# Optimization experiments

Measured on AMD Instinct MI355X. Metric: run time of the kernel, lower is better.

## Reference

```python
import jax, jax.numpy as jnp
import numpy as np

BATCH = 2048          # options['batch_size']; 2B = 4096 rows
D = 512               # projection dim
TAU = 0.1             # options['tau']


def _neg_cols(bs):
    """Column indices of negatives per row, matching sim[mask].view(2bs, -1).

    mask excludes the main diagonal and the +/- bs off-diagonals; each row
    keeps 2bs-2 columns, in ascending (row-major) order.
    """
    n = 2 * bs
    mask = ~(np.eye(n, dtype=bool)
             | np.eye(n, k=bs, dtype=bool)
             | np.eye(n, k=-bs, dtype=bool))
    cols = np.nonzero(mask)[1].reshape(n, n - 2).astype(np.int32)
    return cols

_NEG_COLS = _neg_cols(BATCH)  # static (2B, 2B-2) int32 constant


def setup_inputs() -> dict:
    key = jax.random.key(0)
    representation = jax.random.normal(key, (2 * BATCH, D), dtype=jnp.float32)
    return {"representation": representation}


def reference(representation):
    bs = representation.shape[0] // 2
    # dot-product similarity (options['cosine_similarity'] == False)
    sim = representation @ representation.T                     # (2B, 2B)
    l_pos = jnp.diagonal(sim, offset=bs)                        # (B,)
    r_pos = jnp.diagonal(sim, offset=-bs)                       # (B,)
    positives = jnp.concatenate([l_pos, r_pos])[:, None]        # (2B, 1)
    negatives = jnp.take_along_axis(sim, jnp.asarray(_NEG_COLS), axis=1)  # (2B, 2B-2)
    logits = jnp.concatenate([positives, negatives], axis=1) / TAU
    # CrossEntropyLoss(reduction='sum') with all labels == 0, then / 2B
    loss = -jax.nn.log_softmax(logits, axis=-1)[:, 0]
    return jnp.sum(loss) / (2 * bs)
```

## Files before the change

### kernel.cpp

```cpp
#include <hip/hip_runtime.h>
#include <hip/hip_bf16.h>


#define NROWS 4096
#define DDIM  512
#define NSPLIT 16
#define NT 8
#define BM 128
#define NEG_BIG (-3.0e38f)
#define SQRT_CSCALE 3.798282562f
#define LN2 0.69314718055994530942f
#define THR 40.0f

typedef __bf16 bf16x8 __attribute__((ext_vector_type(8)));
typedef float  f32x4  __attribute__((ext_vector_type(4)));

#define GLOAD_LDS16(g, l) __builtin_amdgcn_global_load_lds(                    \
    (const __attribute__((address_space(1))) void*)(g),                        \
    (__attribute__((address_space(3))) void*)(l), 16, 0, 0)

#define MFMA16(a, b, c) __builtin_amdgcn_mfma_f32_16x16x32_bf16((a), (b), (c), 0, 0, 0)

__global__ void jl_cvt(const float* __restrict__ in, __bf16* __restrict__ out) {
    int i = (blockIdx.x * 256 + threadIdx.x) * 8;
    float4 a = *(const float4*)(in + i);
    float4 b = *(const float4*)(in + i + 4);
    bf16x8 w;
    w[0] = (__bf16)(a.x * SQRT_CSCALE); w[1] = (__bf16)(a.y * SQRT_CSCALE);
    w[2] = (__bf16)(a.z * SQRT_CSCALE); w[3] = (__bf16)(a.w * SQRT_CSCALE);
    w[4] = (__bf16)(b.x * SQRT_CSCALE); w[5] = (__bf16)(b.y * SQRT_CSCALE);
    w[6] = (__bf16)(b.z * SQRT_CSCALE); w[7] = (__bf16)(b.w * SQRT_CSCALE);
    *(bf16x8*)(out + i) = w;
}

__global__ __launch_bounds__(256, 2) void jl_main(const __bf16* __restrict__ rb,
                                                  float* __restrict__ pm,
                                                  float* __restrict__ ps,
                                                  float* __restrict__ pos) {
    __shared__ __align__(16) char smem[2][32][1024];

    const int rbk  = blockIdx.x >> 4;
    const int q    = blockIdx.x & 15;
    const int wave = threadIdx.x >> 6;
    const int lane = threadIdx.x & 63;

    const int row0 = rbk * BM + wave * 32;
    const int col0 = q * 256;
    const int lrow = lane & 15;
    const int lk   = lane >> 4;
    const int swz  = (lrow & 7) << 4;

    bf16x8 afA[16], afB[16];
    {
        const __bf16* arow = rb + (size_t)(row0 + lrow) * DDIM + lk * 8;
        #pragma unroll
        for (int kb = 0; kb < 16; ++kb) {
            afA[kb] = *(const bf16x8*)(arow + kb * 32);
            afB[kb] = *(const bf16x8*)(arow + 16 * DDIM + kb * 32);
        }
    }

#define STAGE(J)                                                               \
    do {                                                                       \
        _Pragma("unroll")                                                      \
        for (int i_ = 0; i_ < 8; ++i_) {                                       \
            const int rl_ = wave * 8 + i_;                                     \
            const char* g_ = (const char*)(rb + (size_t)(col0 + (J) * 32 + rl_) * DDIM) \
                             + ((lane * 16) ^ ((rl_ & 7) << 4));               \
            GLOAD_LDS16(g_, &smem[(J) & 1][rl_][0]);                           \
        }                                                                      \
    } while (0)

    STAGE(0);

    float m[2][4], s[2][4];
    #pragma unroll
    for (int h = 0; h < 2; ++h)
        #pragma unroll
        for (int r = 0; r < 4; ++r) { m[h][r] = NEG_BIG; s[h][r] = 0.0f; }

    for (int jt = 0; jt < NT; ++jt) {
        asm volatile("s_waitcnt vmcnt(0)" ::: "memory");
        __builtin_amdgcn_s_barrier();
        __builtin_amdgcn_sched_barrier(0);
        if (jt + 1 < NT) STAGE(jt + 1);

        const int cb = jt & 1;

        f32x4 a00 = {0.f,0.f,0.f,0.f}, a01 = {0.f,0.f,0.f,0.f};
        f32x4 a10 = {0.f,0.f,0.f,0.f}, a11 = {0.f,0.f,0.f,0.f};
        __builtin_amdgcn_s_setprio(1);
        #pragma unroll
        for (int kb = 0; kb < 16; ++kb) {
            bf16x8 b0 = *(const bf16x8*)(&smem[cb][lrow][0]      + ((kb * 64 + lk * 16) ^ swz));
            bf16x8 b1 = *(const bf16x8*)(&smem[cb][16 + lrow][0] + ((kb * 64 + lk * 16) ^ swz));
            a00 = MFMA16(afA[kb], b0, a00);
            a10 = MFMA16(afB[kb], b0, a10);
            a01 = MFMA16(afA[kb], b1, a01);
            a11 = MFMA16(afB[kb], b1, a11);
        }
        __builtin_amdgcn_s_setprio(0);

        f32x4 y[2][2] = {{a00, a01}, {a10, a11}};
        const int ctile = col0 + jt * 32;

        if (ctile == (row0 ^ 2048)) {
            #pragma unroll
            for (int h = 0; h < 2; ++h)
                #pragma unroll
                for (int r = 0; r < 4; ++r)
                    if (lrow == 4 * lk + r)
                        pos[row0 + h * 16 + 4 * lk + r] = y[h][h][r];
        }

        if (ctile == row0) {
            #pragma unroll
            for (int h = 0; h < 2; ++h)
                #pragma unroll
                for (int r = 0; r < 4; ++r) {
                    if (lrow == 4 * lk + r) y[h][h][r] = NEG_BIG;
                    float y0 = y[h][0][r], y1 = y[h][1][r];
                    float mn = fmaxf(m[h][r], fmaxf(y0, y1));
                    s[h][r] = s[h][r] * __builtin_amdgcn_exp2f(m[h][r] - mn)
                            + __builtin_amdgcn_exp2f(y0 - mn)
                            + __builtin_amdgcn_exp2f(y1 - mn);
                    m[h][r] = mn;
                }
        } else {
            float t[2][2][4];
            float dmax = NEG_BIG;
            #pragma unroll
            for (int h = 0; h < 2; ++h)
                #pragma unroll
                for (int n = 0; n < 2; ++n)
                    #pragma unroll
                    for (int r = 0; r < 4; ++r) {
                        t[h][n][r] = y[h][n][r] - m[h][r];
                        dmax = fmaxf(dmax, t[h][n][r]);
                    }
            if (__any(dmax > THR)) {
                #pragma unroll
                for (int h = 0; h < 2; ++h)
                    #pragma unroll
                    for (int r = 0; r < 4; ++r) {
                        float y0 = y[h][0][r], y1 = y[h][1][r];
                        float mn = fmaxf(m[h][r], fmaxf(y0, y1));
                        s[h][r] = s[h][r] * __builtin_amdgcn_exp2f(m[h][r] - mn)
                                + __builtin_amdgcn_exp2f(y0 - mn)
                                + __builtin_amdgcn_exp2f(y1 - mn);
                        m[h][r] = mn;
                    }
            } else {
                #pragma unroll
                for (int h = 0; h < 2; ++h)
                    #pragma unroll
                    for (int r = 0; r < 4; ++r)
                        s[h][r] += __builtin_amdgcn_exp2f(t[h][0][r])
                                 + __builtin_amdgcn_exp2f(t[h][1][r]);
            }
        }
    }
#undef STAGE

    #pragma unroll
    for (int h = 0; h < 2; ++h)
        #pragma unroll
        for (int r = 0; r < 4; ++r) {
            float mm = m[h][r], ss = s[h][r];
            #pragma unroll
            for (int off = 1; off < 16; off <<= 1) {
                float mo = __shfl_xor(mm, off, 64);
                float so = __shfl_xor(ss, off, 64);
                float mn = fmaxf(mm, mo);
                ss = ss * __builtin_amdgcn_exp2f(mm - mn)
                   + so * __builtin_amdgcn_exp2f(mo - mn);
                mm = mn;
            }
            if (lrow == 0) {
                const int grow = row0 + 16 * h + 4 * lk + r;
                pm[grow * NSPLIT + q] = mm;
                ps[grow * NSPLIT + q] = ss;
            }
        }
}

__global__ void jl_rowloss(const float* __restrict__ pm, const float* __restrict__ ps,
                           const float* __restrict__ pos, float* __restrict__ part) {
    __shared__ float red[256];
    const int t = threadIdx.x;
    const int row = blockIdx.x * 256 + t;
    float mb = NEG_BIG;
    #pragma unroll
    for (int qq = 0; qq < NSPLIT; ++qq) mb = fmaxf(mb, pm[row * NSPLIT + qq]);
    float st = 0.0f;
    #pragma unroll
    for (int qq = 0; qq < NSPLIT; ++qq)
        st += ps[row * NSPLIT + qq] * __builtin_amdgcn_exp2f(pm[row * NSPLIT + qq] - mb);
    red[t] = mb + __builtin_amdgcn_logf(st) - pos[row];
    __syncthreads();
    for (int off = 128; off > 0; off >>= 1) {
        if (t < off) red[t] += red[t + off];
        __syncthreads();
    }
    if (t == 0) part[blockIdx.x] = red[0];
}

__global__ void jl_final(const float* __restrict__ part, float* __restrict__ out) {
    const int t = threadIdx.x;
    float v = (t < NROWS / 256) ? part[t] : 0.0f;
    #pragma unroll
    for (int off = 1; off < 16; off <<= 1) v += __shfl_xor(v, off, 64);
    if (t == 0) out[0] = v * (LN2 / (float)NROWS);
}

extern "C" void kernel_launch(void* const* d_in, const int* in_sizes, int n_in,
                              void* d_out, int out_size, void* d_ws, size_t ws_size,
                              hipStream_t stream) {
    const float* rep = (const float*)d_in[0];
    float* out = (float*)d_out;

    __bf16* rbuf = (__bf16*)d_ws;
    float*  pm   = (float*)(rbuf + (size_t)NROWS * DDIM);
    float*  ps   = pm + NROWS * NSPLIT;
    float*  pos  = ps + NROWS * NSPLIT;
    float*  part = pos + NROWS;

    jl_cvt<<<(NROWS * DDIM) / (256 * 8), 256, 0, stream>>>(rep, rbuf);
    jl_main<<<32 * NSPLIT, 256, 0, stream>>>(rbuf, pm, ps, pos);
    jl_rowloss<<<NROWS / 256, 256, 0, stream>>>(pm, ps, pos, part);
    jl_final<<<1, 64, 0, stream>>>(part, out);
}
```

Measured before the change: 42.01 us.

## Restructure main kernel into 256x256 block tiles with K-streamed LDS staging

The main kernel switches from 128-row blocks that hold A fragments in registers and stream 32-column B tiles to 512-thread blocks computing full 256x256 output tiles. Both A and B are staged through double-buffered LDS in 64-wide K chunks, and each wave accumulates a 128x64 sub-tile. The online softmax now runs once after accumulation instead of per column tile. This raises arithmetic intensity per LDS byte and removes the per-tile softmax bookkeeping, at the cost of 128 accumulator registers per thread, 128 KB of LDS, extra barriers, and four times as many partial (max, sum) slots for the row-reduction kernel.

```diff
diff --git a/kernel.cpp b/kernel.cpp
--- a/kernel.cpp
+++ b/kernel.cpp
@@ -4,13 +4,10 @@
 
 #define NROWS 4096
 #define DDIM  512
-#define NSPLIT 16
-#define NT 8
-#define BM 128
+#define NSLOT 64
 #define NEG_BIG (-3.0e38f)
 #define SQRT_CSCALE 3.798282562f
 #define LN2 0.69314718055994530942f
-#define THR 40.0f
 
 typedef __bf16 bf16x8 __attribute__((ext_vector_type(8)));
 typedef float  f32x4  __attribute__((ext_vector_type(4)));
@@ -33,155 +30,137 @@
     *(bf16x8*)(out + i) = w;
 }
 
-__global__ __launch_bounds__(256, 2) void jl_main(const __bf16* __restrict__ rb,
+__global__ __launch_bounds__(512, 2) void jl_main(const __bf16* __restrict__ rb,
                                                   float* __restrict__ pm,
                                                   float* __restrict__ ps,
                                                   float* __restrict__ pos) {
-    __shared__ __align__(16) char smem[2][32][1024];
+    __shared__ __align__(16) char lds[2][2][256 * 128];
 
     const int rbk  = blockIdx.x >> 4;
     const int q    = blockIdx.x & 15;
     const int wave = threadIdx.x >> 6;
     const int lane = threadIdx.x & 63;
-
-    const int row0 = rbk * BM + wave * 32;
-    const int col0 = q * 256;
+    const int wr   = wave >> 2;
+    const int wc   = wave & 3;
     const int lrow = lane & 15;
     const int lk   = lane >> 4;
-    const int swz  = (lrow & 7) << 4;
-
-    bf16x8 afA[16], afB[16];
-    {
-        const __bf16* arow = rb + (size_t)(row0 + lrow) * DDIM + lk * 8;
+
+    const int row0 = rbk * 256;
+    const int col0 = q * 256;
+    const char* rbb = (const char*)rb;
+
+    const int srow = wave * 32 + (lane >> 3);
+    const int ssw  = ((lane & 7) << 4) ^ (((lane >> 3) & 7) << 4);
+    const char* gA = rbb + (size_t)(row0 + srow) * 1024 + ssw;
+    const char* gB = rbb + (size_t)(col0 + srow) * 1024 + ssw;
+
+#define STAGEP(T, i)                                                           \
+    do {                                                                       \
+        GLOAD_LDS16(gA + (size_t)(T) * 128 + (i) * 8192,                       \
+                    &lds[(T) & 1][0][(wave * 32 + 8 * (i)) * 128]);            \
+        GLOAD_LDS16(gB + (size_t)(T) * 128 + (i) * 8192,                       \
+                    &lds[(T) & 1][1][(wave * 32 + 8 * (i)) * 128]);            \
+    } while (0)
+
+    const int rswz = (lrow & 7) << 4;
+#define AOFF(fr, kb) (((wr * 128 + (fr) * 16 + lrow) * 128) + ((((kb) * 64) + lk * 16) ^ rswz))
+#define BOFF(fc, kb) (((wc * 64 + (fc) * 16 + lrow) * 128) + ((((kb) * 64) + lk * 16) ^ rswz))
+
+    f32x4 acc[8][4];
+    #pragma unroll
+    for (int fr = 0; fr < 8; ++fr)
         #pragma unroll
-        for (int kb = 0; kb < 16; ++kb) {
-            afA[kb] = *(const bf16x8*)(arow + kb * 32);
-            afB[kb] = *(const bf16x8*)(arow + 16 * DDIM + kb * 32);
-        }
-    }
-
-#define STAGE(J)                                                               \
-    do {                                                                       \
-        _Pragma("unroll")                                                      \
-        for (int i_ = 0; i_ < 8; ++i_) {                                       \
-            const int rl_ = wave * 8 + i_;                                     \
-            const char* g_ = (const char*)(rb + (size_t)(col0 + (J) * 32 + rl_) * DDIM) \
-                             + ((lane * 16) ^ ((rl_ & 7) << 4));               \
-            GLOAD_LDS16(g_, &smem[(J) & 1][rl_][0]);                           \
-        }                                                                      \
-    } while (0)
-
-    STAGE(0);
-
-    float m[2][4], s[2][4];
-    #pragma unroll
-    for (int h = 0; h < 2; ++h)
-        #pragma unroll
-        for (int r = 0; r < 4; ++r) { m[h][r] = NEG_BIG; s[h][r] = 0.0f; }
-
-    for (int jt = 0; jt < NT; ++jt) {
+        for (int fc = 0; fc < 4; ++fc)
+            acc[fr][fc] = (f32x4){0.f, 0.f, 0.f, 0.f};
+
+    #pragma unroll
+    for (int i = 0; i < 4; ++i) STAGEP(0, i);
+
+    for (int t = 0; t < 8; ++t) {
         asm volatile("s_waitcnt vmcnt(0)" ::: "memory");
         __builtin_amdgcn_s_barrier();
         __builtin_amdgcn_sched_barrier(0);
-        if (jt + 1 < NT) STAGE(jt + 1);
-
-        const int cb = jt & 1;
-
-        f32x4 a00 = {0.f,0.f,0.f,0.f}, a01 = {0.f,0.f,0.f,0.f};
-        f32x4 a10 = {0.f,0.f,0.f,0.f}, a11 = {0.f,0.f,0.f,0.f};
-        __builtin_amdgcn_s_setprio(1);
+
+        const char* ldsA = &lds[t & 1][0][0];
+        const char* ldsB = &lds[t & 1][1][0];
+        bf16x8 bfr[4][2];
+
         #pragma unroll
-        for (int kb = 0; kb < 16; ++kb) {
-            bf16x8 b0 = *(const bf16x8*)(&smem[cb][lrow][0]      + ((kb * 64 + lk * 16) ^ swz));
-            bf16x8 b1 = *(const bf16x8*)(&smem[cb][16 + lrow][0] + ((kb * 64 + lk * 16) ^ swz));
-            a00 = MFMA16(afA[kb], b0, a00);
-            a10 = MFMA16(afB[kb], b0, a10);
-            a01 = MFMA16(afA[kb], b1, a01);
-            a11 = MFMA16(afB[kb], b1, a11);
-        }
-        __builtin_amdgcn_s_setprio(0);
-
-        f32x4 y[2][2] = {{a00, a01}, {a10, a11}};
-        const int ctile = col0 + jt * 32;
-
-        if (ctile == (row0 ^ 2048)) {
+        for (int p = 0; p < 4; ++p) {
+            if (p == 0) {
+                #pragma unroll
+                for (int fc = 0; fc < 4; ++fc) {
+                    bfr[fc][0] = *(const bf16x8*)(ldsB + BOFF(fc, 0));
+                    bfr[fc][1] = *(const bf16x8*)(ldsB + BOFF(fc, 1));
+                }
+            }
+            bf16x8 a00 = *(const bf16x8*)(ldsA + AOFF(2 * p,     0));
+            bf16x8 a01 = *(const bf16x8*)(ldsA + AOFF(2 * p,     1));
+            bf16x8 a10 = *(const bf16x8*)(ldsA + AOFF(2 * p + 1, 0));
+            bf16x8 a11 = *(const bf16x8*)(ldsA + AOFF(2 * p + 1, 1));
+
+            if (p < 2 && t < 7) {
+                STAGEP(t + 1, 2 * p);
+                STAGEP(t + 1, 2 * p + 1);
+            }
+
+            __builtin_amdgcn_s_barrier();
+            asm volatile("s_waitcnt lgkmcnt(0)" ::: "memory");
+            __builtin_amdgcn_sched_barrier(0);
+
+            __builtin_amdgcn_s_setprio(1);
             #pragma unroll
-            for (int h = 0; h < 2; ++h)
-                #pragma unroll
-                for (int r = 0; r < 4; ++r)
-                    if (lrow == 4 * lk + r)
-                        pos[row0 + h * 16 + 4 * lk + r] = y[h][h][r];
-        }
-
-        if (ctile == row0) {
-            #pragma unroll
-            for (int h = 0; h < 2; ++h)
-                #pragma unroll
-                for (int r = 0; r < 4; ++r) {
-                    if (lrow == 4 * lk + r) y[h][h][r] = NEG_BIG;
-                    float y0 = y[h][0][r], y1 = y[h][1][r];
-                    float mn = fmaxf(m[h][r], fmaxf(y0, y1));
-                    s[h][r] = s[h][r] * __builtin_amdgcn_exp2f(m[h][r] - mn)
-                            + __builtin_amdgcn_exp2f(y0 - mn)
-                            + __builtin_amdgcn_exp2f(y1 - mn);
-                    m[h][r] = mn;
-                }
-        } else {
-            float t[2][2][4];
-            float dmax = NEG_BIG;
-            #pragma unroll
-            for (int h = 0; h < 2; ++h)
-                #pragma unroll
-                for (int n = 0; n < 2; ++n)
-                    #pragma unroll
-                    for (int r = 0; r < 4; ++r) {
-                        t[h][n][r] = y[h][n][r] - m[h][r];
-                        dmax = fmaxf(dmax, t[h][n][r]);
-                    }
-            if (__any(dmax > THR)) {
-                #pragma unroll
-                for (int h = 0; h < 2; ++h)
-                    #pragma unroll
-                    for (int r = 0; r < 4; ++r) {
-                        float y0 = y[h][0][r], y1 = y[h][1][r];
-                        float mn = fmaxf(m[h][r], fmaxf(y0, y1));
-                        s[h][r] = s[h][r] * __builtin_amdgcn_exp2f(m[h][r] - mn)
-                                + __builtin_amdgcn_exp2f(y0 - mn)
-                                + __builtin_amdgcn_exp2f(y1 - mn);
-                        m[h][r] = mn;
-                    }
-            } else {
-                #pragma unroll
-                for (int h = 0; h < 2; ++h)
-                    #pragma unroll
-                    for (int r = 0; r < 4; ++r)
-                        s[h][r] += __builtin_amdgcn_exp2f(t[h][0][r])
-                                 + __builtin_amdgcn_exp2f(t[h][1][r]);
-            }
+            for (int fc = 0; fc < 4; ++fc) {
+                acc[2 * p][fc]     = MFMA16(a00, bfr[fc][0], acc[2 * p][fc]);
+                acc[2 * p][fc]     = MFMA16(a01, bfr[fc][1], acc[2 * p][fc]);
+                acc[2 * p + 1][fc] = MFMA16(a10, bfr[fc][0], acc[2 * p + 1][fc]);
+                acc[2 * p + 1][fc] = MFMA16(a11, bfr[fc][1], acc[2 * p + 1][fc]);
+            }
+            __builtin_amdgcn_s_setprio(0);
+            __builtin_amdgcn_s_barrier();
         }
     }
-#undef STAGE
-
-    #pragma unroll
-    for (int h = 0; h < 2; ++h)
+#undef STAGEP
+
+    const bool isdiag = (rbk == q);
+    const bool ispos  = (q == (rbk ^ 8));
+
+    #pragma unroll
+    for (int fr = 0; fr < 8; ++fr) {
         #pragma unroll
         for (int r = 0; r < 4; ++r) {
-            float mm = m[h][r], ss = s[h][r];
+            const int rr = wr * 128 + fr * 16 + 4 * lk + r;
+            float v0 = acc[fr][0][r], v1 = acc[fr][1][r];
+            float v2 = acc[fr][2][r], v3 = acc[fr][3][r];
+            if (ispos | isdiag) {
+                const int cb = wc * 64 + lrow;
+                #pragma unroll
+                for (int fc = 0; fc < 4; ++fc) {
+                    float* vp = (fc == 0) ? &v0 : (fc == 1) ? &v1 : (fc == 2) ? &v2 : &v3;
+                    if (cb + fc * 16 == rr) {
+                        if (ispos) pos[row0 + rr] = *vp;
+                        if (isdiag) *vp = NEG_BIG;
+                    }
+                }
+            }
+            float mm = fmaxf(fmaxf(v0, v1), fmaxf(v2, v3));
+            float ss = __builtin_amdgcn_exp2f(v0 - mm) + __builtin_amdgcn_exp2f(v1 - mm)
+                     + __builtin_amdgcn_exp2f(v2 - mm) + __builtin_amdgcn_exp2f(v3 - mm);
             #pragma unroll
             for (int off = 1; off < 16; off <<= 1) {
                 float mo = __shfl_xor(mm, off, 64);
                 float so = __shfl_xor(ss, off, 64);
                 float mn = fmaxf(mm, mo);
-                ss = ss * __builtin_amdgcn_exp2f(mm - mn)
-                   + so * __builtin_amdgcn_exp2f(mo - mn);
+                ss = ss * __builtin_amdgcn_exp2f(mm - mn) + so * __builtin_amdgcn_exp2f(mo - mn);
                 mm = mn;
             }
             if (lrow == 0) {
-                const int grow = row0 + 16 * h + 4 * lk + r;
-                pm[grow * NSPLIT + q] = mm;
-                ps[grow * NSPLIT + q] = ss;
+                const int grow = row0 + rr;
+                pm[grow * NSLOT + q * 4 + wc] = mm;
+                ps[grow * NSLOT + q * 4 + wc] = ss;
             }
         }
+    }
 }
 
 __global__ void jl_rowloss(const float* __restrict__ pm, const float* __restrict__ ps,
@@ -190,12 +169,10 @@
     const int t = threadIdx.x;
     const int row = blockIdx.x * 256 + t;
     float mb = NEG_BIG;
-    #pragma unroll
-    for (int qq = 0; qq < NSPLIT; ++qq) mb = fmaxf(mb, pm[row * NSPLIT + qq]);
+    for (int qq = 0; qq < NSLOT; ++qq) mb = fmaxf(mb, pm[row * NSLOT + qq]);
     float st = 0.0f;
-    #pragma unroll
-    for (int qq = 0; qq < NSPLIT; ++qq)
-        st += ps[row * NSPLIT + qq] * __builtin_amdgcn_exp2f(pm[row * NSPLIT + qq] - mb);
+    for (int qq = 0; qq < NSLOT; ++qq)
+        st += ps[row * NSLOT + qq] * __builtin_amdgcn_exp2f(pm[row * NSLOT + qq] - mb);
     red[t] = mb + __builtin_amdgcn_logf(st) - pos[row];
     __syncthreads();
     for (int off = 128; off > 0; off >>= 1) {
@@ -221,12 +198,12 @@
 
     __bf16* rbuf = (__bf16*)d_ws;
     float*  pm   = (float*)(rbuf + (size_t)NROWS * DDIM);
-    float*  ps   = pm + NROWS * NSPLIT;
-    float*  pos  = ps + NROWS * NSPLIT;
+    float*  ps   = pm + (size_t)NROWS * NSLOT;
+    float*  pos  = ps + (size_t)NROWS * NSLOT;
     float*  part = pos + NROWS;
 
     jl_cvt<<<(NROWS * DDIM) / (256 * 8), 256, 0, stream>>>(rep, rbuf);
-    jl_main<<<32 * NSPLIT, 256, 0, stream>>>(rbuf, pm, ps, pos);
+    jl_main<<<16 * 16, 512, 0, stream>>>(rbuf, pm, ps, pos);
     jl_rowloss<<<NROWS / 256, 256, 0, stream>>>(pm, ps, pos, part);
     jl_final<<<1, 64, 0, stream>>>(part, out);
 }
```

New measurement: 49.13 us. +17.0%, slower.

## Exploit Gram matrix symmetry: compute upper-triangle tiles only with column-wise partial softmax

Applied to the files above, without the earlier changes.

The similarity matrix is symmetric, so the main kernel now processes only the 528 upper-triangular 128x128 block tiles instead of all 1024. Off-diagonal tiles emit both row-wise and column-wise partial log-sum-exp statistics into a 128-slot per-row buffer, and positives are written for both mirrored rows. The row-loss kernel merges the variable set of slots per row. This roughly halves the MFMA work, but adds cross-lane column reductions, more exps per tile, and more scattered partial writes and reads.

```diff
diff --git a/kernel.cpp b/kernel.cpp
--- a/kernel.cpp
+++ b/kernel.cpp
@@ -4,9 +4,8 @@
 
 #define NROWS 4096
 #define DDIM  512
-#define NSPLIT 16
-#define NT 8
-#define BM 128
+#define NSLOT 128
+#define NT 4
 #define NEG_BIG (-3.0e38f)
 #define SQRT_CSCALE 3.798282562f
 #define LN2 0.69314718055994530942f
@@ -39,16 +38,18 @@
                                                   float* __restrict__ pos) {
     __shared__ __align__(16) char smem[2][32][1024];
 
-    const int rbk  = blockIdx.x >> 4;
-    const int q    = blockIdx.x & 15;
+    int br = 0, rem = blockIdx.x;
+    while (rem >= 32 - br) { rem -= 32 - br; ++br; }
+    const int bc = br + rem;
+
     const int wave = threadIdx.x >> 6;
     const int lane = threadIdx.x & 63;
-
-    const int row0 = rbk * BM + wave * 32;
-    const int col0 = q * 256;
+    const int row0 = br * 128 + wave * 32;
+    const int colb = bc * 128;
     const int lrow = lane & 15;
     const int lk   = lane >> 4;
     const int swz  = (lrow & 7) << 4;
+    const char* rbb = (const char*)rb;
 
     bf16x8 afA[16], afB[16];
     {
@@ -63,11 +64,11 @@
 #define STAGE(J)                                                               \
     do {                                                                       \
         _Pragma("unroll")                                                      \
-        for (int i_ = 0; i_ < 8; ++i_) {                                       \
-            const int rl_ = wave * 8 + i_;                                     \
-            const char* g_ = (const char*)(rb + (size_t)(col0 + (J) * 32 + rl_) * DDIM) \
-                             + ((lane * 16) ^ ((rl_ & 7) << 4));               \
-            GLOAD_LDS16(g_, &smem[(J) & 1][rl_][0]);                           \
+        for (int j_ = 0; j_ < 8; ++j_) {                                       \
+            const int rr_ = wave * 8 + j_;                                     \
+            const char* g_ = rbb + (size_t)(colb + (J) * 32 + rr_) * 1024      \
+                             + ((lane * 16) ^ ((rr_ & 7) << 4));               \
+            GLOAD_LDS16(g_, &smem[(J) & 1][rr_][0]);                           \
         }                                                                      \
     } while (0)
 
@@ -86,7 +87,6 @@
         if (jt + 1 < NT) STAGE(jt + 1);
 
         const int cb = jt & 1;
-
         f32x4 a00 = {0.f,0.f,0.f,0.f}, a01 = {0.f,0.f,0.f,0.f};
         f32x4 a10 = {0.f,0.f,0.f,0.f}, a11 = {0.f,0.f,0.f,0.f};
         __builtin_amdgcn_s_setprio(1);
@@ -102,31 +102,30 @@
         __builtin_amdgcn_s_setprio(0);
 
         f32x4 y[2][2] = {{a00, a01}, {a10, a11}};
-        const int ctile = col0 + jt * 32;
+        const int ctile = colb + jt * 32;
 
         if (ctile == (row0 ^ 2048)) {
             #pragma unroll
             for (int h = 0; h < 2; ++h)
                 #pragma unroll
                 for (int r = 0; r < 4; ++r)
-                    if (lrow == 4 * lk + r)
-                        pos[row0 + h * 16 + 4 * lk + r] = y[h][h][r];
-        }
-
-        if (ctile == row0) {
+                    if (lrow == 4 * lk + r) {
+                        const int grow = row0 + h * 16 + 4 * lk + r;
+                        float v = y[h][h][r];
+                        pos[grow] = v;
+                        pos[grow ^ 2048] = v;
+                    }
+        }
+
+        if (br == bc && ctile == row0) {
             #pragma unroll
             for (int h = 0; h < 2; ++h)
                 #pragma unroll
-                for (int r = 0; r < 4; ++r) {
+                for (int r = 0; r < 4; ++r)
                     if (lrow == 4 * lk + r) y[h][h][r] = NEG_BIG;
-                    float y0 = y[h][0][r], y1 = y[h][1][r];
-                    float mn = fmaxf(m[h][r], fmaxf(y0, y1));
-                    s[h][r] = s[h][r] * __builtin_amdgcn_exp2f(m[h][r] - mn)
-                            + __builtin_amdgcn_exp2f(y0 - mn)
-                            + __builtin_amdgcn_exp2f(y1 - mn);
-                    m[h][r] = mn;
-                }
-        } else {
+        }
+
+        {
             float t[2][2][4];
             float dmax = NEG_BIG;
             #pragma unroll
@@ -159,6 +158,38 @@
                                  + __builtin_amdgcn_exp2f(t[h][1][r]);
             }
         }
+
+        if (br != bc) {
+            #pragma unroll
+            for (int fc = 0; fc < 2; ++fc) {
+                float cm = NEG_BIG;
+                #pragma unroll
+                for (int h = 0; h < 2; ++h)
+                    #pragma unroll
+                    for (int r = 0; r < 4; ++r)
+                        cm = fmaxf(cm, y[h][fc][r]);
+                float cs = 0.0f;
+                #pragma unroll
+                for (int h = 0; h < 2; ++h)
+                    #pragma unroll
+                    for (int r = 0; r < 4; ++r)
+                        cs += __builtin_amdgcn_exp2f(y[h][fc][r] - cm);
+                #pragma unroll
+                for (int off = 16; off < 64; off <<= 1) {
+                    float mo = __shfl_xor(cm, off, 64);
+                    float so = __shfl_xor(cs, off, 64);
+                    float mn = fmaxf(cm, mo);
+                    cs = cs * __builtin_amdgcn_exp2f(cm - mn)
+                       + so * __builtin_amdgcn_exp2f(mo - mn);
+                    cm = mn;
+                }
+                if (lane < 16) {
+                    const int gcol = ctile + fc * 16 + lane;
+                    pm[(size_t)gcol * NSLOT + br * 4 + wave] = cm;
+                    ps[(size_t)gcol * NSLOT + br * 4 + wave] = cs;
+                }
+            }
+        }
     }
 #undef STAGE
 
@@ -178,8 +209,8 @@
             }
             if (lrow == 0) {
                 const int grow = row0 + 16 * h + 4 * lk + r;
-                pm[grow * NSPLIT + q] = mm;
-                ps[grow * NSPLIT + q] = ss;
+                pm[(size_t)grow * NSLOT + bc * 4 + wave] = mm;
+                ps[(size_t)grow * NSLOT + bc * 4 + wave] = ss;
             }
         }
 }
@@ -189,13 +220,30 @@
     __shared__ float red[256];
     const int t = threadIdx.x;
     const int row = blockIdx.x * 256 + t;
+    const int bi = row >> 7;
+    const int wi = (row >> 5) & 3;
+    const float* pmr = pm + (size_t)row * NSLOT;
+    const float* psr = ps + (size_t)row * NSLOT;
+
     float mb = NEG_BIG;
-    #pragma unroll
-    for (int qq = 0; qq < NSPLIT; ++qq) mb = fmaxf(mb, pm[row * NSPLIT + qq]);
+    for (int d = 0; d < 32; ++d) {
+        if (d < bi) {
+            #pragma unroll
+            for (int w = 0; w < 4; ++w) mb = fmaxf(mb, pmr[d * 4 + w]);
+        } else {
+            mb = fmaxf(mb, pmr[d * 4 + wi]);
+        }
+    }
     float st = 0.0f;
-    #pragma unroll
-    for (int qq = 0; qq < NSPLIT; ++qq)
-        st += ps[row * NSPLIT + qq] * __builtin_amdgcn_exp2f(pm[row * NSPLIT + qq] - mb);
+    for (int d = 0; d < 32; ++d) {
+        if (d < bi) {
+            #pragma unroll
+            for (int w = 0; w < 4; ++w)
+                st += psr[d * 4 + w] * __builtin_amdgcn_exp2f(pmr[d * 4 + w] - mb);
+        } else {
+            st += psr[d * 4 + wi] * __builtin_amdgcn_exp2f(pmr[d * 4 + wi] - mb);
+        }
+    }
     red[t] = mb + __builtin_amdgcn_logf(st) - pos[row];
     __syncthreads();
     for (int off = 128; off > 0; off >>= 1) {
@@ -221,12 +269,12 @@
 
     __bf16* rbuf = (__bf16*)d_ws;
     float*  pm   = (float*)(rbuf + (size_t)NROWS * DDIM);
-    float*  ps   = pm + NROWS * NSPLIT;
-    float*  pos  = ps + NROWS * NSPLIT;
+    float*  ps   = pm + (size_t)NROWS * NSLOT;
+    float*  pos  = ps + (size_t)NROWS * NSLOT;
     float*  part = pos + NROWS;
 
     jl_cvt<<<(NROWS * DDIM) / (256 * 8), 256, 0, stream>>>(rep, rbuf);
-    jl_main<<<32 * NSPLIT, 256, 0, stream>>>(rbuf, pm, ps, pos);
+    jl_main<<<528, 256, 0, stream>>>(rbuf, pm, ps, pos);
     jl_rowloss<<<NROWS / 256, 256, 0, stream>>>(pm, ps, pos, part);
     jl_final<<<1, 64, 0, stream>>>(part, out);
 }
```

Result: slower. 69.52 us (+65.5%).

## Software-pipeline softmax epilogue one tile behind MFMA accumulation

Applied to the files above, without the earlier changes.

Defers the online-softmax epilogue of each column tile by one iteration, so tile j-1's exp/max work can interleave with tile j's MFMA chain. The jt loop is fully unrolled, and the setprio bracketing around the MFMA loop is removed. This trades more live registers (an extra set of four accumulators) for hiding the epilogue latency behind matrix math, with a risk of higher register pressure and more code.

```diff
diff --git a/kernel.cpp b/kernel.cpp
--- a/kernel.cpp
+++ b/kernel.cpp
@@ -79,6 +79,68 @@
         #pragma unroll
         for (int r = 0; r < 4; ++r) { m[h][r] = NEG_BIG; s[h][r] = 0.0f; }
 
+    f32x4 q00 = {0,0,0,0}, q01 = {0,0,0,0}, q10 = {0,0,0,0}, q11 = {0,0,0,0};
+
+#define EPILOGUE(v00, v01, v10, v11, ct)                                       \
+    do {                                                                       \
+        f32x4 y[2][2] = {{(v00), (v01)}, {(v10), (v11)}};                      \
+        if ((ct) == (row0 ^ 2048)) {                                           \
+            _Pragma("unroll")                                                  \
+            for (int h = 0; h < 2; ++h)                                        \
+                _Pragma("unroll")                                              \
+                for (int r = 0; r < 4; ++r)                                    \
+                    if (lrow == 4 * lk + r)                                    \
+                        pos[row0 + h * 16 + 4 * lk + r] = y[h][h][r];          \
+        }                                                                      \
+        if ((ct) == row0) {                                                    \
+            _Pragma("unroll")                                                  \
+            for (int h = 0; h < 2; ++h)                                        \
+                _Pragma("unroll")                                              \
+                for (int r = 0; r < 4; ++r) {                                  \
+                    if (lrow == 4 * lk + r) y[h][h][r] = NEG_BIG;              \
+                    float y0 = y[h][0][r], y1 = y[h][1][r];                    \
+                    float mn = fmaxf(m[h][r], fmaxf(y0, y1));                  \
+                    s[h][r] = s[h][r] * __builtin_amdgcn_exp2f(m[h][r] - mn)   \
+                            + __builtin_amdgcn_exp2f(y0 - mn)                  \
+                            + __builtin_amdgcn_exp2f(y1 - mn);                 \
+                    m[h][r] = mn;                                              \
+                }                                                              \
+        } else {                                                               \
+            float tv[2][2][4];                                                 \
+            float dmax = NEG_BIG;                                              \
+            _Pragma("unroll")                                                  \
+            for (int h = 0; h < 2; ++h)                                        \
+                _Pragma("unroll")                                              \
+                for (int n = 0; n < 2; ++n)                                    \
+                    _Pragma("unroll")                                          \
+                    for (int r = 0; r < 4; ++r) {                              \
+                        tv[h][n][r] = y[h][n][r] - m[h][r];                    \
+                        dmax = fmaxf(dmax, tv[h][n][r]);                       \
+                    }                                                          \
+            if (__any(dmax > THR)) {                                           \
+                _Pragma("unroll")                                              \
+                for (int h = 0; h < 2; ++h)                                    \
+                    _Pragma("unroll")                                          \
+                    for (int r = 0; r < 4; ++r) {                              \
+                        float y0 = y[h][0][r], y1 = y[h][1][r];                \
+                        float mn = fmaxf(m[h][r], fmaxf(y0, y1));              \
+                        s[h][r] = s[h][r] * __builtin_amdgcn_exp2f(m[h][r] - mn) \
+                                + __builtin_amdgcn_exp2f(y0 - mn)              \
+                                + __builtin_amdgcn_exp2f(y1 - mn);             \
+                        m[h][r] = mn;                                          \
+                    }                                                          \
+            } else {                                                           \
+                _Pragma("unroll")                                              \
+                for (int h = 0; h < 2; ++h)                                    \
+                    _Pragma("unroll")                                          \
+                    for (int r = 0; r < 4; ++r)                                \
+                        s[h][r] += __builtin_amdgcn_exp2f(tv[h][0][r])         \
+                                 + __builtin_amdgcn_exp2f(tv[h][1][r]);        \
+            }                                                                  \
+        }                                                                      \
+    } while (0)
+
+    #pragma unroll
     for (int jt = 0; jt < NT; ++jt) {
         asm volatile("s_waitcnt vmcnt(0)" ::: "memory");
         __builtin_amdgcn_s_barrier();
@@ -89,7 +151,6 @@
 
         f32x4 a00 = {0.f,0.f,0.f,0.f}, a01 = {0.f,0.f,0.f,0.f};
         f32x4 a10 = {0.f,0.f,0.f,0.f}, a11 = {0.f,0.f,0.f,0.f};
-        __builtin_amdgcn_s_setprio(1);
         #pragma unroll
         for (int kb = 0; kb < 16; ++kb) {
             bf16x8 b0 = *(const bf16x8*)(&smem[cb][lrow][0]      + ((kb * 64 + lk * 16) ^ swz));
@@ -99,68 +160,15 @@
             a01 = MFMA16(afA[kb], b1, a01);
             a11 = MFMA16(afB[kb], b1, a11);
         }
-        __builtin_amdgcn_s_setprio(0);
-
-        f32x4 y[2][2] = {{a00, a01}, {a10, a11}};
-        const int ctile = col0 + jt * 32;
-
-        if (ctile == (row0 ^ 2048)) {
-            #pragma unroll
-            for (int h = 0; h < 2; ++h)
-                #pragma unroll
-                for (int r = 0; r < 4; ++r)
-                    if (lrow == 4 * lk + r)
-                        pos[row0 + h * 16 + 4 * lk + r] = y[h][h][r];
-        }
-
-        if (ctile == row0) {
-            #pragma unroll
-            for (int h = 0; h < 2; ++h)
-                #pragma unroll
-                for (int r = 0; r < 4; ++r) {
-                    if (lrow == 4 * lk + r) y[h][h][r] = NEG_BIG;
-                    float y0 = y[h][0][r], y1 = y[h][1][r];
-                    float mn = fmaxf(m[h][r], fmaxf(y0, y1));
-                    s[h][r] = s[h][r] * __builtin_amdgcn_exp2f(m[h][r] - mn)
-                            + __builtin_amdgcn_exp2f(y0 - mn)
-                            + __builtin_amdgcn_exp2f(y1 - mn);
-                    m[h][r] = mn;
-                }
-        } else {
-            float t[2][2][4];
-            float dmax = NEG_BIG;
-            #pragma unroll
-            for (int h = 0; h < 2; ++h)
-                #pragma unroll
-                for (int n = 0; n < 2; ++n)
-                    #pragma unroll
-                    for (int r = 0; r < 4; ++r) {
-                        t[h][n][r] = y[h][n][r] - m[h][r];
-                        dmax = fmaxf(dmax, t[h][n][r]);
-                    }
-            if (__any(dmax > THR)) {
-                #pragma unroll
-                for (int h = 0; h < 2; ++h)
-                    #pragma unroll
-                    for (int r = 0; r < 4; ++r) {
-                        float y0 = y[h][0][r], y1 = y[h][1][r];
-                        float mn = fmaxf(m[h][r], fmaxf(y0, y1));
-                        s[h][r] = s[h][r] * __builtin_amdgcn_exp2f(m[h][r] - mn)
-                                + __builtin_amdgcn_exp2f(y0 - mn)
-                                + __builtin_amdgcn_exp2f(y1 - mn);
-                        m[h][r] = mn;
-                    }
-            } else {
-                #pragma unroll
-                for (int h = 0; h < 2; ++h)
-                    #pragma unroll
-                    for (int r = 0; r < 4; ++r)
-                        s[h][r] += __builtin_amdgcn_exp2f(t[h][0][r])
-                                 + __builtin_amdgcn_exp2f(t[h][1][r]);
-            }
-        }
+
+        if (jt > 0) {
+            EPILOGUE(q00, q01, q10, q11, col0 + (jt - 1) * 32);
+        }
+        q00 = a00; q01 = a01; q10 = a10; q11 = a11;
     }
+    EPILOGUE(q00, q01, q10, q11, col0 + (NT - 1) * 32);
 #undef STAGE
+#undef EPILOGUE
 
     #pragma unroll
     for (int h = 0; h < 2; ++h)
```

After: 42.03 us. About the same (+0.1%).
